# Optimization experiments

Measured on AMD Instinct MI355X. Metric: run time of the kernel, lower is better.

## Reference

```python
import jax, jax.numpy as jnp
import numpy as np

B, N, T, C, H, K = 2, 32, 512, 64, 4, 3
PAD = K - 1  # causal left-padding along time
HD = C // H


def setup_inputs() -> dict:
    key = jax.random.key(0)
    ks = jax.random.split(key, 9)
    s = 1.0 / np.sqrt(C)
    return {
        "values": jax.random.normal(ks[0], (B, N, T, C), jnp.float32),
        "keys": jax.random.normal(ks[1], (B, N, T, C), jnp.float32),
        "query": jax.random.normal(ks[2], (B, N, T, C), jnp.float32),
        "Wq": jax.random.normal(ks[3], (C, C, K, 1), jnp.float32) * s,  # Conv2d (out,in,k,1)
        "bq": jax.random.normal(ks[4], (C,), jnp.float32) * s,
        "Wk": jax.random.normal(ks[5], (C, C, K, 1), jnp.float32) * s,
        "bk": jax.random.normal(ks[6], (C,), jnp.float32) * s,
        "Wv": jax.random.normal(ks[7], (C, C), jnp.float32) * s,  # 1x1 conv, no bias
        "Wf": jax.random.normal(ks[8], (C, C), jnp.float32) * s,  # Linear (out,in)
        "bf": jnp.zeros((C,), jnp.float32),
    }


def _causal_conv(x, w, b):
    # x: (B,N,T,C) -> NCHW (B,C,T,N); kernel (k,1) over T with left pad = K-1 (causal)
    xp = jnp.transpose(x, (0, 3, 2, 1))
    y = jax.lax.conv_general_dilated(
        xp, w, window_strides=(1, 1), padding=[(PAD, 0), (0, 0)],
        dimension_numbers=("NCHW", "OIHW", "NCHW"))
    y = y + b[None, :, None, None]
    return jnp.transpose(y, (0, 3, 2, 1))  # back to (B,N,T,C)


def reference(values, keys, query, Wq, bq, Wk, bk, Wv, Wf, bf):
    q = _causal_conv(query, Wq, bq).reshape(B, N, T, H, HD)
    k = _causal_conv(keys, Wk, bk).reshape(B, N, T, H, HD)
    v = jnp.einsum("bntc,oc->bnto", values, Wv).reshape(B, N, T, H, HD)  # 1x1 conv
    energy = jnp.einsum("bnqhd,bnkhd->bnqkh", q, k)  # (B,N,T,T,H)
    attn = jax.nn.softmax(energy / np.sqrt(C).astype(np.float32), axis=3)
    out = jnp.einsum("bnqkh,bnkhd->bnqhd", attn, v).reshape(B, N, T, C)
    return out @ Wf.T + bf
```

## Files before the change

### kernel.cpp

```cpp
#include <hip/hip_runtime.h>

#define DEVI __device__ __forceinline__

typedef __attribute__((ext_vector_type(8)))  short s16x8;
typedef __attribute__((ext_vector_type(4)))  short s16x4;
typedef __attribute__((ext_vector_type(4)))  float f32x4;
typedef __attribute__((ext_vector_type(16))) float f32x16;
typedef __attribute__((ext_vector_type(2)))  unsigned u32x2;
typedef __attribute__((ext_vector_type(4)))  unsigned u32x4;

DEVI short f2bf(float f) {
  unsigned u = __builtin_bit_cast(unsigned, f);
  u = u + 0x7fffu + ((u >> 16) & 1u);
  return (short)(u >> 16);
}
DEVI unsigned cvtpk(float lo, float hi) {
  unsigned r;
  asm("v_cvt_pk_bf16_f32 %0, %1, %2" : "=v"(r) : "v"(lo), "v"(hi));
  return r;
}
DEVI void gll16(const short* g, short* l) {
  __builtin_amdgcn_global_load_lds(
      (const __attribute__((address_space(1))) unsigned*)g,
      (__attribute__((address_space(3))) unsigned*)l, 16, 0, 0);
}

constexpr int TT = 512;
constexpr int CC = 64;
constexpr float SCLQ = 0.18033688011112042f;

__global__ __launch_bounds__(256) void k_qkv(const float* __restrict__ values,
                                             const float* __restrict__ keys,
                                             const float* __restrict__ query,
                                             const float* __restrict__ Wq,
                                             const float* __restrict__ bq,
                                             const float* __restrict__ Wk,
                                             const float* __restrict__ bk,
                                             const float* __restrict__ Wv,
                                             short* __restrict__ qg,
                                             short* __restrict__ kg,
                                             short* __restrict__ vgT) {
  __shared__ __align__(16) short smem[16896];
  short* lx = smem;
  const int idx = blockIdx.x;
  const int xcd = idx & 7, rest = idx >> 3;
  const int tsr = rest >> 6;
  const int rr = rest & 63;
  const int bn = xcd * 8 + (rr >> 3), t8 = rr & 7;
  const int t0 = t8 * 64;
  const size_t xbase = (size_t)bn * TT * CC;
  const int tid = threadIdx.x;
  const int lane = tid & 63, w = tid >> 6;
  const int r = lane & 31, hl = lane >> 5;

  const float* in = (tsr == 0) ? query : (tsr == 1) ? keys : values;
  const int nrows = (tsr < 2) ? 66 : 64;
  const int halo = (tsr < 2) ? 2 : 0;
  short* lw = (tsr < 2) ? (smem + 4224) : (smem + 8320);
  short* lxT = smem + 4224;

  if (tsr < 2) {
    const float* wsrc = tsr ? Wk : Wq;
    for (int s = tid; s < 4096; s += 256) {
      lw[s]        = f2bf(wsrc[s * 3 + 0]);
      lw[4096 + s] = f2bf(wsrc[s * 3 + 1]);
      lw[8192 + s] = f2bf(wsrc[s * 3 + 2]);
    }
  } else {
    for (int s = tid; s < 4096; s += 256) lw[s] = f2bf(Wv[s]);
  }

  for (int s = tid; s < nrows * 8; s += 256) {
    int row = s >> 3, c8 = s & 7;
    int t = t0 - halo + row;
    u32x4 rv;
    if (t >= 0) {
      const float4 a = *(const float4*)(in + xbase + (size_t)t * 64 + c8 * 8);
      const float4 b = *(const float4*)(in + xbase + (size_t)t * 64 + c8 * 8 + 4);
      rv[0] = cvtpk(a.x, a.y); rv[1] = cvtpk(a.z, a.w);
      rv[2] = cvtpk(b.x, b.y); rv[3] = cvtpk(b.z, b.w);
    } else {
      rv = (u32x4)(0u);
    }
    int byte = row * 128 + ((c8 * 16) ^ ((row & 7) << 4));
    *(u32x4*)((char*)lx + byte) = rv;
  }
  __syncthreads();

  {
    int mt = w >> 1, nt = w & 1;
    f32x16 acc;
#pragma unroll
    for (int i = 0; i < 16; ++i) acc[i] = 0.f;

    if (tsr < 2) {
#pragma unroll
      for (int kk = 0; kk < 3; ++kk) {
#pragma unroll
        for (int c4 = 0; c4 < 4; ++c4) {
          int lrow = mt * 32 + r + kk;
          int abyte = lrow * 128 + (((c4 * 16 + hl * 8) * 2) ^ ((lrow & 7) << 4));
          s16x8 af = *(const s16x8*)((const char*)lx + abyte);
          s16x8 bfr = *(const s16x8*)(lw + kk * 4096 + (nt * 32 + r) * 64 + c4 * 16 + hl * 8);
          acc = __builtin_amdgcn_mfma_f32_32x32x16_bf16(af, bfr, acc, 0, 0, 0);
        }
      }
    } else {
#pragma unroll
      for (int c4 = 0; c4 < 4; ++c4) {
        int lrow = mt * 32 + r;
        int abyte = lrow * 128 + (((c4 * 16 + hl * 8) * 2) ^ ((lrow & 7) << 4));
        s16x8 af = *(const s16x8*)((const char*)lx + abyte);
        s16x8 bfr = *(const s16x8*)(lw + (nt * 32 + r) * 64 + c4 * 16 + hl * 8);
        acc = __builtin_amdgcn_mfma_f32_32x32x16_bf16(af, bfr, acc, 0, 0, 0);
      }
    }
    int co = nt * 32 + r;
    if (tsr == 2) {
#pragma unroll
      for (int g2 = 0; g2 < 4; ++g2) {
        int tl = mt * 32 + g2 * 8 + hl * 4;
        u32x2 pk;
        pk[0] = cvtpk(acc[g2 * 4 + 0], acc[g2 * 4 + 1]);
        pk[1] = cvtpk(acc[g2 * 4 + 2], acc[g2 * 4 + 3]);
        *(u32x2*)(lxT + co * 64 + (tl ^ ((co & 15) << 2))) = pk;
      }
    } else {
      float bias = tsr ? bk[co] : bq[co];
      float scl = tsr ? 1.f : SCLQ;
      short* dst = tsr ? kg : qg;
#pragma unroll
      for (int reg = 0; reg < 16; ++reg) {
        int trow = mt * 32 + (reg & 3) + 8 * (reg >> 2) + 4 * hl;
        dst[((size_t)bn * TT + (t0 + trow)) * 64 + co] = f2bf((acc[reg] + bias) * scl);
      }
    }
  }
  if (tsr == 2) {
    __syncthreads();
#pragma unroll
    for (int i = 0; i < 4; ++i) {
      int chunk = tid + 256 * i;
      int co = chunk >> 4, tc = chunk & 15;
      s16x4 v4 = *(const s16x4*)(lxT + co * 64 + ((tc * 4) ^ ((co & 15) << 2)));
      *(s16x4*)(vgT + ((size_t)bn * 64 + co) * TT + t0 + tc * 4) = v4;
    }
  }
}

__global__ __launch_bounds__(256, 4) void k_attn(const short* __restrict__ qg,
                                                 const short* __restrict__ kg,
                                                 const short* __restrict__ vgT,
                                                 short* __restrict__ ag) {
  __shared__ __align__(16) short Kl[512 * 16];
  __shared__ __align__(16) short Vl[16 * 512];
  __shared__ float Sums[4][32];
  const int tid = threadIdx.x;
  const int b = (blockIdx.x & 7) * 128 + (blockIdx.x >> 3);
  const int bn = b >> 4, h = (b >> 2) & 3, qq = b & 3;
  const int lane = tid & 63, w = tid >> 6;
  const int r = lane & 31, hl = lane >> 5;

  const short* kslice = kg + (size_t)bn * TT * CC + h * 16;
#pragma unroll
  for (int j = 0; j < 4; ++j) {
    int g = j * 256 + tid;
    int nt = g >> 6, l = g & 63;
    gll16(kslice + (size_t)(nt * 32 + (l & 31)) * 64 + (l >> 5) * 8, Kl + g * 8);
  }
  const short* vslice = vgT + ((size_t)bn * 64 + h * 16) * TT;
#pragma unroll
  for (int j = 0; j < 4; ++j) {
    int d = j * 256 + tid;
    int ch = d >> 6, tc = (d & 63) ^ (ch & 7);
    gll16(vslice + (size_t)ch * TT + tc * 8, Vl + d * 8);
  }

  const int mt = qq * 4 + w;
  s16x8 qf = *(const s16x8*)(qg + ((size_t)bn * TT + mt * 32 + r) * CC + h * 16 + hl * 8);
  const int vch = r & 15;
  const char* vrow = (const char*)Vl + vch * 1024;

  __syncthreads();

  f32x16 z;
#pragma unroll
  for (int i = 0; i < 16; ++i) z[i] = 0.f;
  float sm0 = 0.f, sm1 = 0.f, sm2 = 0.f, sm3 = 0.f;
  f32x16 o;
#pragma unroll
  for (int i = 0; i < 16; ++i) o[i] = 0.f;

#pragma unroll
  for (int nt = 0; nt < 16; ++nt) {
    s16x8 kf = *(const s16x8*)(Kl + nt * 512 + lane * 8);
    f32x16 s = __builtin_amdgcn_mfma_f32_32x32x16_bf16(kf, qf, z, 0, 0, 0);
    float p[16];
#pragma unroll
    for (int i = 0; i < 16; ++i)
      p[i] = fmaxf(__builtin_amdgcn_exp2f(s[i]), 0.f);
#pragma unroll
    for (int i = 0; i < 4; ++i) {
      sm0 += p[4 * i + 0]; sm1 += p[4 * i + 1];
      sm2 += p[4 * i + 2]; sm3 += p[4 * i + 3];
    }
    unsigned pk[8];
#pragma unroll
    for (int m = 0; m < 8; ++m) pk[m] = cvtpk(p[2 * m], p[2 * m + 1]);
#pragma unroll
    for (int s2 = 0; s2 < 2; ++s2) {
      unsigned a0 = pk[4 * s2 + 0], b0 = pk[4 * s2 + 2];
      unsigned a1 = pk[4 * s2 + 1], b1 = pk[4 * s2 + 3];
      asm("v_permlane32_swap_b32 %0, %1" : "+v"(a0), "+v"(b0));
      asm("v_permlane32_swap_b32 %0, %1" : "+v"(a1), "+v"(b1));
      u32x4 fw; fw[0] = a0; fw[1] = a1; fw[2] = b0; fw[3] = b1;
      s16x8 fr = __builtin_bit_cast(s16x8, fw);
      s16x8 vf = *(const s16x8*)(vrow + (((nt * 32 + s2 * 16 + hl * 8) * 2) ^ ((vch & 7) << 4)));
      o = __builtin_amdgcn_mfma_f32_32x32x16_bf16(fr, vf, o, 0, 0, 0);
    }
  }
  float sum = (sm0 + sm1) + (sm2 + sm3);
  sum += __shfl_xor(sum, 32);
  Sums[w][r] = sum;
  if (r < 16) {
#pragma unroll
    for (int reg = 0; reg < 16; ++reg) {
      int qlocal = (reg & 3) + 8 * (reg >> 2) + 4 * hl;
      float inv = __builtin_amdgcn_rcpf(Sums[w][qlocal]);
      int q = mt * 32 + qlocal;
      ag[((size_t)bn * TT + q) * CC + h * 16 + r] = f2bf(o[reg] * inv);
    }
  }
}

__global__ __launch_bounds__(256) void k_out(const short* __restrict__ ag,
                                             const float* __restrict__ Wf,
                                             const float* __restrict__ bfv,
                                             float* __restrict__ out) {
  __shared__ __align__(16) short la[64 * 64];
  __shared__ __align__(16) short lw[64 * 64];
  const int tid = threadIdx.x;
  const int xcd = blockIdx.x & 7, rest = blockIdx.x >> 3;
  const int bn = xcd * 8 + (rest >> 3), t8 = rest & 7;
  const int t0 = t8 * 64;
#pragma unroll
  for (int j = 0; j < 2; ++j) {
    int d = j * 256 + tid;
    int row = d >> 3, c8 = (d & 7) ^ (row & 7);
    gll16(ag + ((size_t)bn * TT + t0 + row) * 64 + c8 * 8, la + d * 8);
  }
  for (int s = tid; s < 4096; s += 256) lw[s] = f2bf(Wf[s]);
  __syncthreads();
  const int lane = tid & 63, w = tid >> 6;
  const int r = lane & 31, hl = lane >> 5;
  {
    int mt = w >> 1, nt = w & 1;
    f32x16 acc;
#pragma unroll
    for (int i = 0; i < 16; ++i) acc[i] = 0.f;
#pragma unroll
    for (int c4 = 0; c4 < 4; ++c4) {
      int lrow = mt * 32 + r;
      int abyte = lrow * 128 + (((c4 * 16 + hl * 8) * 2) ^ ((lrow & 7) << 4));
      s16x8 af = *(const s16x8*)((const char*)la + abyte);
      s16x8 bfr = *(const s16x8*)(lw + (nt * 32 + r) * 64 + c4 * 16 + hl * 8);
      acc = __builtin_amdgcn_mfma_f32_32x32x16_bf16(af, bfr, acc, 0, 0, 0);
    }
    int co = nt * 32 + r;
    float bias = bfv[co];
#pragma unroll
    for (int reg = 0; reg < 16; ++reg) {
      int trow = mt * 32 + (reg & 3) + 8 * (reg >> 2) + 4 * hl;
      out[((size_t)bn * TT + t0 + trow) * 64 + co] = acc[reg] + bias;
    }
  }
}

extern "C" void kernel_launch(void* const* d_in, const int* in_sizes, int n_in,
                              void* d_out, int out_size, void* d_ws, size_t ws_size,
                              hipStream_t stream) {
  const float* values = (const float*)d_in[0];
  const float* keys = (const float*)d_in[1];
  const float* query = (const float*)d_in[2];
  const float* Wq = (const float*)d_in[3];
  const float* bq = (const float*)d_in[4];
  const float* Wk = (const float*)d_in[5];
  const float* bk = (const float*)d_in[6];
  const float* Wv = (const float*)d_in[7];
  const float* Wf = (const float*)d_in[8];
  const float* bfv = (const float*)d_in[9];
  float* out = (float*)d_out;

  char* ws = (char*)d_ws;
  short* qg = (short*)ws;
  short* kg = (short*)(ws + (1 << 22));
  short* vgT = (short*)(ws + 2 * (1 << 22));
  short* ag = (short*)(ws + 3 * (size_t)(1 << 22));

  hipLaunchKernelGGL(k_qkv, dim3(1536), dim3(256), 0, stream,
                     values, keys, query, Wq, bq, Wk, bk, Wv, qg, kg, vgT);
  hipLaunchKernelGGL(k_attn, dim3(1024), dim3(256), 0, stream, qg, kg, vgT, ag);
  hipLaunchKernelGGL(k_out, dim3(512), dim3(256), 0, stream, ag, Wf, bfv, out);
}
```

Before: 37.91 us.

## Store K in MFMA-fragment layout and read it directly from global memory

```diff
diff --git a/kernel.cpp b/kernel.cpp
--- a/kernel.cpp
+++ b/kernel.cpp
@@ -38,7 +38,7 @@
                                              const float* __restrict__ bk,
                                              const float* __restrict__ Wv,
                                              short* __restrict__ qg,
-                                             short* __restrict__ kg,
+                                             short* __restrict__ kgF,
                                              short* __restrict__ vgT) {
   __shared__ __align__(16) short smem[16896];
   short* lx = smem;
@@ -125,14 +125,21 @@
         pk[1] = cvtpk(acc[g2 * 4 + 2], acc[g2 * 4 + 3]);
         *(u32x2*)(lxT + co * 64 + (tl ^ ((co & 15) << 2))) = pk;
       }
-    } else {
-      float bias = tsr ? bk[co] : bq[co];
-      float scl = tsr ? 1.f : SCLQ;
-      short* dst = tsr ? kg : qg;
+    } else if (tsr == 0) {
+      float bias = bq[co];
 #pragma unroll
       for (int reg = 0; reg < 16; ++reg) {
         int trow = mt * 32 + (reg & 3) + 8 * (reg >> 2) + 4 * hl;
-        dst[((size_t)bn * TT + (t0 + trow)) * 64 + co] = f2bf((acc[reg] + bias) * scl);
+        qg[((size_t)bn * TT + (t0 + trow)) * 64 + co] = f2bf((acc[reg] + bias) * SCLQ);
+      }
+    } else {
+      float bias = bk[co];
+      int h = co >> 4, ch = co & 15;
+      short* kb = kgF + ((size_t)bn * 4 + h) * 8192 + (ch >> 3) * 256 + (ch & 7);
+#pragma unroll
+      for (int reg = 0; reg < 16; ++reg) {
+        int t = t0 + mt * 32 + (reg & 3) + 8 * (reg >> 2) + 4 * hl;
+        kb[(t >> 5) * 512 + (t & 31) * 8] = f2bf(acc[reg] + bias);
       }
     }
   }
@@ -149,10 +156,9 @@
 }
 
 __global__ __launch_bounds__(256, 4) void k_attn(const short* __restrict__ qg,
-                                                 const short* __restrict__ kg,
+                                                 const short* __restrict__ kgF,
                                                  const short* __restrict__ vgT,
                                                  short* __restrict__ ag) {
-  __shared__ __align__(16) short Kl[512 * 16];
   __shared__ __align__(16) short Vl[16 * 512];
   __shared__ float Sums[4][32];
   const int tid = threadIdx.x;
@@ -161,13 +167,6 @@
   const int lane = tid & 63, w = tid >> 6;
   const int r = lane & 31, hl = lane >> 5;
 
-  const short* kslice = kg + (size_t)bn * TT * CC + h * 16;
-#pragma unroll
-  for (int j = 0; j < 4; ++j) {
-    int g = j * 256 + tid;
-    int nt = g >> 6, l = g & 63;
-    gll16(kslice + (size_t)(nt * 32 + (l & 31)) * 64 + (l >> 5) * 8, Kl + g * 8);
-  }
   const short* vslice = vgT + ((size_t)bn * 64 + h * 16) * TT;
 #pragma unroll
   for (int j = 0; j < 4; ++j) {
@@ -178,6 +177,7 @@
 
   const int mt = qq * 4 + w;
   s16x8 qf = *(const s16x8*)(qg + ((size_t)bn * TT + mt * 32 + r) * CC + h * 16 + hl * 8);
+  const short* kgh = kgF + ((size_t)bn * 4 + h) * 8192 + lane * 8;
   const int vch = r & 15;
   const char* vrow = (const char*)Vl + vch * 1024;
 
@@ -193,7 +193,7 @@
 
 #pragma unroll
   for (int nt = 0; nt < 16; ++nt) {
-    s16x8 kf = *(const s16x8*)(Kl + nt * 512 + lane * 8);
+    s16x8 kf = *(const s16x8*)(kgh + nt * 512);
     f32x16 s = __builtin_amdgcn_mfma_f32_32x32x16_bf16(kf, qf, z, 0, 0, 0);
     float p[16];
 #pragma unroll
@@ -293,12 +293,12 @@
 
   char* ws = (char*)d_ws;
   short* qg = (short*)ws;
-  short* kg = (short*)(ws + (1 << 22));
+  short* kgF = (short*)(ws + (1 << 22));
   short* vgT = (short*)(ws + 2 * (1 << 22));
   short* ag = (short*)(ws + 3 * (size_t)(1 << 22));
 
   hipLaunchKernelGGL(k_qkv, dim3(1536), dim3(256), 0, stream,
-                     values, keys, query, Wq, bq, Wk, bk, Wv, qg, kg, vgT);
-  hipLaunchKernelGGL(k_attn, dim3(1024), dim3(256), 0, stream, qg, kg, vgT, ag);
+                     values, keys, query, Wq, bq, Wk, bk, Wv, qg, kgF, vgT);
+  hipLaunchKernelGGL(k_attn, dim3(1024), dim3(256), 0, stream, qg, kgF, vgT, ag);
   hipLaunchKernelGGL(k_out, dim3(512), dim3(256), 0, stream, ag, Wf, bfv, out);
 }
```

Measured after the change: 38.47 us. No clear change (+1.5%).
